# Optimization experiments

Hardware: AMD Instinct MI355X
Metric: run time of the kernel (lower is better)

The kernel has to match this reference:

```python
import jax, jax.numpy as jnp
import numpy as np
from jax import lax

B, T = 64, 256
V, E, H, O = 50000, 256, 512, 50

def _xavier(key, shape):
    fan_in, fan_out = shape[1], shape[0]
    std = float(np.sqrt(2.0 / (fan_in + fan_out)))
    return jax.random.normal(key, shape, dtype=jnp.float32) * std

def lstm_scan(x, W_ih, W_hh, b, h0, c0):
    # x: (B, T, Din); precompute input projection for all timesteps
    xg = jnp.einsum('btd,gd->btg', x, W_ih) + b  # (B, T, 4H)
    def step(carry, xg_t):
        h, c = carry
        g = xg_t + h @ W_hh.T
        i, f, gg, o = jnp.split(g, 4, axis=-1)
        i = jax.nn.sigmoid(i); f = jax.nn.sigmoid(f)
        gg = jnp.tanh(gg); o = jax.nn.sigmoid(o)
        c = f * c + i * gg
        h = o * jnp.tanh(c)
        return (h, c), h
    _, hs = lax.scan(step, (h0, c0), jnp.transpose(xg, (1, 0, 2)))
    return jnp.transpose(hs, (1, 0, 2))  # (B, T, H)

def bilstm(x, W_ih, W_hh, b, h0, c0):
    # Faithful to source bugs: output_backward == output_forward flipped on BATCH dim
    out_f = lstm_scan(x, W_ih, W_hh, b, h0, c0)
    return jnp.concatenate([out_f, out_f[::-1]], axis=-1)  # (B, T, 2H)

def setup_inputs() -> dict:
    key = jax.random.key(0)
    ks = jax.random.split(key, 14)
    x = jax.random.randint(ks[0], (B, T), 0, V + 1, dtype=jnp.int32)
    emb = jax.random.normal(ks[1], (V + 1, E), dtype=jnp.float32)
    emb = emb.at[0].set(0.0)  # padding_idx=0
    s = 1.0 / np.sqrt(H)
    W_ih1 = jax.random.uniform(ks[2], (4 * H, E), minval=-s, maxval=s, dtype=jnp.float32)
    W_hh1 = jax.random.uniform(ks[3], (4 * H, H), minval=-s, maxval=s, dtype=jnp.float32)
    b1 = jax.random.uniform(ks[4], (4 * H,), minval=-s, maxval=s, dtype=jnp.float32)
    W_ih2 = jax.random.uniform(ks[5], (4 * H, 2 * H), minval=-s, maxval=s, dtype=jnp.float32)
    W_hh2 = jax.random.uniform(ks[6], (4 * H, H), minval=-s, maxval=s, dtype=jnp.float32)
    b2 = jax.random.uniform(ks[7], (4 * H,), minval=-s, maxval=s, dtype=jnp.float32)
    h01 = _xavier(ks[8], (B, H)); c01 = _xavier(ks[9], (B, H))
    h02 = _xavier(ks[10], (B, H)); c02 = _xavier(ks[11], (B, H))
    Wfc = jax.random.normal(ks[12], (O, 2 * H), dtype=jnp.float32) * 0.02
    bfc = jnp.zeros((O,), dtype=jnp.float32)
    return {"x": x, "emb": emb, "W_ih1": W_ih1, "W_hh1": W_hh1, "b1": b1,
            "h01": h01, "c01": c01, "W_ih2": W_ih2, "W_hh2": W_hh2, "b2": b2,
            "h02": h02, "c02": c02, "Wfc": Wfc, "bfc": bfc}

def reference(x, emb, W_ih1, W_hh1, b1, h01, c01, W_ih2, W_hh2, b2, h02, c02, Wfc, bfc):
    out = emb[x]                                   # (B, T, E) embedding lookup
    out = bilstm(out, W_ih1, W_hh1, b1, h01, c01)  # (B, T, 2H)
    out = bilstm(out, W_ih2, W_hh2, b2, h02, c02)  # (B, T, 2H)
    # dropout is identity at inference
    logits = jnp.einsum('btd,od->bto', out, Wfc) + bfc
    return jax.nn.log_softmax(logits, axis=-1)
```

## Files before the change

kernel.cpp:

```cpp
#include <hip/hip_runtime.h>


#define B_ 64
#define T_ 256
#define E_ 256
#define H_ 512
#define G_ 2048
#define O_ 50
#define NROW (B_ * T_)
#define RING 16

typedef unsigned short u16;
typedef unsigned int u32;
typedef unsigned long long u64;
typedef short bf16x8 __attribute__((ext_vector_type(8)));
typedef u16 u16x4 __attribute__((ext_vector_type(4)));
typedef u32 u32x4 __attribute__((ext_vector_type(4)));
typedef float f32x4 __attribute__((ext_vector_type(4)));

#define LD_AG(p)    __hip_atomic_load((p), __ATOMIC_RELAXED, __HIP_MEMORY_SCOPE_AGENT)
#define ST_AG(p, v) __hip_atomic_store((p), (v), __ATOMIC_RELAXED, __HIP_MEMORY_SCOPE_AGENT)

__device__ __forceinline__ u16 f2bf(float f) {
    unsigned u = __float_as_uint(f);
    return (u16)((u + 0x7fffu + ((u >> 16) & 1u)) >> 16);
}
__device__ __forceinline__ float bf2f(u16 x) {
    return __uint_as_float(((u32)x) << 16);
}
__device__ __forceinline__ float sigm(float x) {
    x = fminf(fmaxf(x, -30.f), 30.f);
    return 1.f / (1.f + __expf(-x));
}
__device__ __forceinline__ float tanh_f(float x) {
    x = fminf(fmaxf(x, -15.f), 15.f);
    float e = __expf(2.f * x);
    return (e - 1.f) / (e + 1.f);
}
__device__ __forceinline__ bf16x8 pack8(const float* p) {
    float4 v0 = *(const float4*)p;
    float4 v1 = *(const float4*)(p + 4);
    bf16x8 bb;
    bb[0] = (short)f2bf(v0.x); bb[1] = (short)f2bf(v0.y);
    bb[2] = (short)f2bf(v0.z); bb[3] = (short)f2bf(v0.w);
    bb[4] = (short)f2bf(v1.x); bb[5] = (short)f2bf(v1.y);
    bb[6] = (short)f2bf(v1.z); bb[7] = (short)f2bf(v1.w);
    return bb;
}


__global__ __launch_bounds__(256) void f32_to_bf16_vec(
    const float* __restrict__ in, u16* __restrict__ out, int n4)
{
    int i = blockIdx.x * 256 + threadIdx.x;
    if (i >= n4) return;
    float4 v = *(const float4*)&in[(size_t)i * 4];
    u16x4 o = { f2bf(v.x), f2bf(v.y), f2bf(v.z), f2bf(v.w) };
    *(u16x4*)&out[(size_t)i * 4] = o;
}

__global__ __launch_bounds__(256) void embed_to_bf16(
    const int* __restrict__ x, const float* __restrict__ emb, u16* __restrict__ A1)
{
    int i = blockIdx.x * 256 + threadIdx.x;
    int r = i >> 6, c4 = (i & 63) * 4;
    int xi = x[r];
    float4 v = *(const float4*)&emb[(size_t)xi * E_ + c4];
    u16x4 o = { f2bf(v.x), f2bf(v.y), f2bf(v.z), f2bf(v.w) };
    *(u16x4*)&A1[(size_t)r * E_ + c4] = o;
}

__global__ __launch_bounds__(256) void wfc_pad(
    const float* __restrict__ Wfc, u16* __restrict__ outp)
{
    int i = blockIdx.x * 256 + threadIdx.x;
    int row = i >> 8, c4 = (i & 255) * 4;
    u16x4 o = { 0, 0, 0, 0 };
    if (row < O_) {
        float4 v = *(const float4*)&Wfc[(size_t)row * 1024 + c4];
        o = u16x4{ f2bf(v.x), f2bf(v.y), f2bf(v.z), f2bf(v.w) };
    }
    *(u16x4*)&outp[(size_t)row * 1024 + c4] = o;
}

__global__ __launch_bounds__(256) void gemm_bf16(
    const u16* __restrict__ A, const u16* __restrict__ Bw,
    const float* __restrict__ bias, u16* __restrict__ C,
    int M, int N, int K)
{
    __shared__ u16 Asm[128][40];
    __shared__ u16 Bsm[128][40];
    const int tid = threadIdx.x, lane = tid & 63, wave = tid >> 6;
    const int wr = wave >> 1, wc = wave & 1;
    const int bm = blockIdx.y, bn = blockIdx.x;
    f32x4 acc[4][4] = {};
    const int r = tid >> 1, kc = (tid & 1) * 16;
    const u16* ag = A  + (size_t)(bm * 128 + r) * K;
    const u16* bg = Bw + (size_t)(bn * 128 + r) * K;
    for (int k0 = 0; k0 < K; k0 += 32) {
        int col = k0 + kc;
        __syncthreads();
        *(int4*)&Asm[r][kc]     = *(const int4*)(ag + col);
        *(int4*)&Asm[r][kc + 8] = *(const int4*)(ag + col + 8);
        *(int4*)&Bsm[r][kc]     = *(const int4*)(bg + col);
        *(int4*)&Bsm[r][kc + 8] = *(const int4*)(bg + col + 8);
        __syncthreads();
        bf16x8 af[4], bf[4];
        #pragma unroll
        for (int mt = 0; mt < 4; mt++)
            af[mt] = *(const bf16x8*)&Asm[wr * 64 + mt * 16 + (lane & 15)][(lane >> 4) * 8];
        #pragma unroll
        for (int nt = 0; nt < 4; nt++)
            bf[nt] = *(const bf16x8*)&Bsm[wc * 64 + nt * 16 + (lane & 15)][(lane >> 4) * 8];
        #pragma unroll
        for (int mt = 0; mt < 4; mt++)
            #pragma unroll
            for (int nt = 0; nt < 4; nt++)
                acc[mt][nt] = __builtin_amdgcn_mfma_f32_16x16x32_bf16(
                    af[mt], bf[nt], acc[mt][nt], 0, 0, 0);
    }
    #pragma unroll
    for (int mt = 0; mt < 4; mt++) {
        #pragma unroll
        for (int nt = 0; nt < 4; nt++) {
            int col = bn * 128 + wc * 64 + nt * 16 + (lane & 15);
            float bv = bias[col];
            #pragma unroll
            for (int rr = 0; rr < 4; rr++) {
                int row = bm * 128 + wr * 64 + mt * 16 + (lane >> 4) * 4 + rr;
                C[(size_t)row * N + col] = f2bf(acc[mt][nt][rr] + bv);
            }
        }
    }
}

__global__ __launch_bounds__(512, 2) void scan12(
    const u16* __restrict__ xgb,
    const float* __restrict__ Whh1,
    const float* __restrict__ h01, const float* __restrict__ c01,
    u32* h1pub,
    u32* hx1,
    const float* __restrict__ Wih2,
    const float* __restrict__ Whh2,
    const float* __restrict__ b2,
    const float* __restrict__ h02, const float* __restrict__ c02,
    u32* ring,
    u32* hx2,
    u32* h2pk,
    int* sents)
{
    __shared__ u16 hl[16][520];
    __shared__ u16 a1cat[16][1032];
    __shared__ float glds[4][8][68];
    const int tid = threadIdx.x, lane = tid & 63, wave = tid >> 6;
    const int idx = blockIdx.x;
    const u64 tmask = 0xffff0000ffff0000ull;
    int budget = 1 << 20;

    if (idx < 64) {
        const int grp = idx & 7, ug = idx >> 3;
        const int gw = wave >> 1, uh = wave & 1;
        for (int j = tid; j < 8 * 260; j += 512) {
            int rw = 8 + j / 260, cl = (j % 260) * 2;
            *(u32*)&hl[rw][cl] = 0;
        }
        bf16x8 breg0[16], breg1[16];
        #pragma unroll
        for (int tt = 0; tt < 2; tt++) {
            const float* wr0 = Whh1
                + (size_t)(gw * H_ + ug * 64 + uh * 32 + tt * 16 + (lane & 15)) * H_
                + ((lane >> 4) * 8);
            #pragma unroll
            for (int kk = 0; kk < 16; kk++) {
                bf16x8 bb = pack8(wr0 + kk * 32);
                if (tt == 0) breg0[kk] = bb; else breg1[kk] = bb;
            }
        }
        const int bb_ = tid >> 6, uu = tid & 63;
        const int brow = grp * 8 + bb_, ucol = ug * 64 + uu;
        float c = c01[brow * H_ + ucol];
        #pragma unroll
        for (int j = 0; j < 8; ++j) {
            int k = tid + j * 512;
            int prow = k >> 9, pcol = k & 511;
            ST_AG(hx1 + (size_t)(grp * 8 + prow) * H_ + pcol,
                  (1u << 16) | (u32)f2bf(h01[(grp * 8 + prow) * H_ + pcol]));
        }
        const int crow = tid >> 6, ccol = (tid & 63) * 8;
        int* mysent = sents + grp * 32 + ug;
        __syncthreads();

        #pragma unroll 1
        for (int t = 0; t < T_; ++t) {
            const size_t xb = ((size_t)brow * T_ + t) * G_ + ucol;
            u16 xi = xgb[xb], xf = xgb[xb + 512];
            u16 xgg = xgb[xb + 1024], xo = xgb[xb + 1536];

            u64* src = (u64*)(hx1 + (size_t)(t & 1) * (B_ * H_)
                              + (size_t)(grp * 8 + crow) * H_ + ccol);
            const u32 wt = (u32)(t + 1);
            const u64 want = ((u64)wt << 16) | ((u64)wt << 48);
            u64 v0 = LD_AG(src + 0), v1 = LD_AG(src + 1);
            u64 v2 = LD_AG(src + 2), v3 = LD_AG(src + 3);
            while ((((v0 ^ want) | (v1 ^ want) | (v2 ^ want) | (v3 ^ want)) & tmask) != 0) {
                if (--budget < 0) break;
                __builtin_amdgcn_s_sleep(1);
                if ((v0 ^ want) & tmask) v0 = LD_AG(src + 0);
                if ((v1 ^ want) & tmask) v1 = LD_AG(src + 1);
                if ((v2 ^ want) & tmask) v2 = LD_AG(src + 2);
                if ((v3 ^ want) & tmask) v3 = LD_AG(src + 3);
            }
            u32x4 pk = { (u32)(v0 & 0xffff) | ((u32)(v0 >> 32) << 16),
                         (u32)(v1 & 0xffff) | ((u32)(v1 >> 32) << 16),
                         (u32)(v2 & 0xffff) | ((u32)(v2 >> 32) << 16),
                         (u32)(v3 & 0xffff) | ((u32)(v3 >> 32) << 16) };
            *(u32x4*)&hl[crow][ccol] = pk;
            __syncthreads();

            f32x4 a0 = {0,0,0,0}, a1 = {0,0,0,0}, a2 = {0,0,0,0}, a3 = {0,0,0,0};
            const int ar = lane & 15, ac = (lane >> 4) * 8;
            #pragma unroll
            for (int kk = 0; kk < 16; kk += 2) {
                bf16x8 f0 = *(const bf16x8*)&hl[ar][ac + kk * 32];
                bf16x8 f1 = *(const bf16x8*)&hl[ar][ac + (kk + 1) * 32];
                a0 = __builtin_amdgcn_mfma_f32_16x16x32_bf16(f0, breg0[kk],     a0, 0, 0, 0);
                a1 = __builtin_amdgcn_mfma_f32_16x16x32_bf16(f1, breg0[kk + 1], a1, 0, 0, 0);
                a2 = __builtin_amdgcn_mfma_f32_16x16x32_bf16(f0, breg1[kk],     a2, 0, 0, 0);
                a3 = __builtin_amdgcn_mfma_f32_16x16x32_bf16(f1, breg1[kk + 1], a3, 0, 0, 0);
            }
            #pragma unroll
            for (int rr = 0; rr < 4; rr++) {
                int br = (lane >> 4) * 4 + rr;
                if (br < 8) {
                    glds[gw][br][uh * 32 + (lane & 15)]      = a0[rr] + a1[rr];
                    glds[gw][br][uh * 32 + 16 + (lane & 15)] = a2[rr] + a3[rr];
                }
            }
            __syncthreads();

            float ip = glds[0][bb_][uu] + bf2f(xi);
            float fp = glds[1][bb_][uu] + bf2f(xf);
            float gp = glds[2][bb_][uu] + bf2f(xgg);
            float op = glds[3][bb_][uu] + bf2f(xo);
            float gi = sigm(ip), gf = sigm(fp), gc = tanh_f(gp), go = sigm(op);
            c = gf * c + gi * gc;
            float h = go * tanh_f(c);
            u32 me = f2bf(h);
            ST_AG(hx1 + (size_t)((t + 1) & 1) * (B_ * H_) + (size_t)brow * H_ + ucol,
                  ((u32)(t + 2) << 16) | me);
            u32 ot = (u32)__shfl_xor((int)me, 1);
            if (!(uu & 1))
                ST_AG(h1pub + ((size_t)brow * T_ + t) * 256 + (ucol >> 1),
                      me | (ot << 16));
            if (tid == 0) ST_AG(mysent, t + 1);
        }
        __syncthreads();
        if (tid == 0) ST_AG(mysent, T_ + 1);

    } else if (idx < 192) {
        const int bg = idx & 7, gg = (idx - 64) >> 3;
        for (int j = tid; j < 8 * 516; j += 512) {
            int rw = 8 + j / 516, cl = (j % 516) * 2;
            *(u32*)&a1cat[rw][cl] = 0;
        }
        const int gcol = gg * 128 + wave * 16 + (lane & 15);
        bf16x8 bi[32];
        {
            const float* wr0 = Wih2 + (size_t)gcol * 1024 + ((lane >> 4) * 8);
            #pragma unroll
            for (int kk = 0; kk < 32; kk++) bi[kk] = pack8(wr0 + kk * 32);
        }
        const float bias = b2[gcol];
        const int crow = tid >> 6, ccol = (tid & 63) * 16;
        const int myb  = bg * 8 + crow;
        const int myfb = (7 - bg) * 8 + (7 - crow);
        const u32* __restrict__ hbase =
            h1pub + (size_t)((ccol < 512) ? myb : myfb) * T_ * 256;
        const int  cadj  = (ccol < 512) ? (ccol >> 1) : ((ccol - 512) >> 1);
        __syncthreads();

        #pragma unroll 1
        for (int t = 0; t < T_; ++t) {
            if (tid < 16) {
                int g2 = (tid < 8) ? bg : (7 - bg);
                int* sp = sents + g2 * 32 + (tid & 7);
                const int want = t + 2;
                while (LD_AG(sp) < want) {
                    if (--budget < 0) break;
                    __builtin_amdgcn_s_sleep(2);
                }
            } else if (tid < 24 && t >= RING) {
                int* sp = sents + 512 + bg * 32 + (tid - 16);
                const int want = t - (RING - 1);
                while (LD_AG(sp) < want) {
                    if (--budget < 0) break;
                    __builtin_amdgcn_s_sleep(2);
                }
            }
            __syncthreads();

            const u32* s0 = hbase + (size_t)t * 256 + cadj;
            u32x4 q0 = *(const u32x4*)(s0);
            u32x4 q1 = *(const u32x4*)(s0 + 4);
            *(u32x4*)&a1cat[crow][ccol]     = q0;
            *(u32x4*)&a1cat[crow][ccol + 8] = q1;
            __syncthreads();

            f32x4 a0 = {0,0,0,0}, a1 = {0,0,0,0}, a2 = {0,0,0,0}, a3 = {0,0,0,0};
            const int ar = lane & 15, ac = (lane >> 4) * 8;
            #pragma unroll
            for (int kk = 0; kk < 32; kk += 4) {
                bf16x8 f0 = *(const bf16x8*)&a1cat[ar][ac + kk * 32];
                bf16x8 f1 = *(const bf16x8*)&a1cat[ar][ac + (kk + 1) * 32];
                bf16x8 f2 = *(const bf16x8*)&a1cat[ar][ac + (kk + 2) * 32];
                bf16x8 f3 = *(const bf16x8*)&a1cat[ar][ac + (kk + 3) * 32];
                a0 = __builtin_amdgcn_mfma_f32_16x16x32_bf16(f0, bi[kk],     a0, 0, 0, 0);
                a1 = __builtin_amdgcn_mfma_f32_16x16x32_bf16(f1, bi[kk + 1], a1, 0, 0, 0);
                a2 = __builtin_amdgcn_mfma_f32_16x16x32_bf16(f2, bi[kk + 2], a2, 0, 0, 0);
                a3 = __builtin_amdgcn_mfma_f32_16x16x32_bf16(f3, bi[kk + 3], a3, 0, 0, 0);
            }
            #pragma unroll
            for (int rr = 0; rr < 4; rr++) {
                int br = (lane >> 4) * 4 + rr;
                u32 me = f2bf((a0[rr] + a1[rr]) + (a2[rr] + a3[rr]) + bias);
                u32 ot = (u32)__shfl_xor((int)me, 1);
                if (br < 8 && !(lane & 1))
                    ST_AG(ring + ((size_t)(t & (RING - 1)) * B_ + bg * 8 + br) * 1024
                          + (gcol >> 1), me | (ot << 16));
            }
            __syncthreads();
            if (tid == 0) ST_AG(sents + 256 + bg * 32 + gg, t + 1);
        }

    } else {
        const int bg = idx & 7, ug = (idx - 192) >> 3;
        const int gw = wave >> 1, uh = wave & 1;
        for (int j = tid; j < 8 * 260; j += 512) {
            int rw = 8 + j / 260, cl = (j % 260) * 2;
            *(u32*)&hl[rw][cl] = 0;
        }
        bf16x8 breg0[16], breg1[16];
        #pragma unroll
        for (int tt = 0; tt < 2; tt++) {
            const float* wr0 = Whh2
                + (size_t)(gw * H_ + ug * 64 + uh * 32 + tt * 16 + (lane & 15)) * H_
                + ((lane >> 4) * 8);
            #pragma unroll
            for (int kk = 0; kk < 16; kk++) {
                bf16x8 bb = pack8(wr0 + kk * 32);
                if (tt == 0) breg0[kk] = bb; else breg1[kk] = bb;
            }
        }
        const int bb_ = tid >> 6, uu = tid & 63;
        const int brow = bg * 8 + bb_, ucol = ug * 64 + uu;
        float c = c02[brow * H_ + ucol];
        #pragma unroll
        for (int j = 0; j < 8; ++j) {
            int k = tid + j * 512;
            int prow = k >> 9, pcol = k & 511;
            ST_AG(hx2 + (size_t)(bg * 8 + prow) * H_ + pcol,
                  (1u << 16) | (u32)f2bf(h02[(bg * 8 + prow) * H_ + pcol]));
        }
        const int crow = tid >> 6, ccol = (tid & 63) * 8;
        __syncthreads();

        #pragma unroll 1
        for (int t = 0; t < T_; ++t) {
            if (tid < 16) {
                int* sp = sents + 256 + bg * 32 + tid;
                const int want = t + 1;
                while (LD_AG(sp) < want) {
                    if (--budget < 0) break;
                    __builtin_amdgcn_s_sleep(2);
                }
            }
            u64* src = (u64*)(hx2 + (size_t)(t & 1) * (B_ * H_)
                              + (size_t)(bg * 8 + crow) * H_ + ccol);
            const u32 wt = (u32)(t + 1);
            const u64 want = ((u64)wt << 16) | ((u64)wt << 48);
            u64 v0 = LD_AG(src + 0), v1 = LD_AG(src + 1);
            u64 v2 = LD_AG(src + 2), v3 = LD_AG(src + 3);
            while ((((v0 ^ want) | (v1 ^ want) | (v2 ^ want) | (v3 ^ want)) & tmask) != 0) {
                if (--budget < 0) break;
                __builtin_amdgcn_s_sleep(1);
                if ((v0 ^ want) & tmask) v0 = LD_AG(src + 0);
                if ((v1 ^ want) & tmask) v1 = LD_AG(src + 1);
                if ((v2 ^ want) & tmask) v2 = LD_AG(src + 2);
                if ((v3 ^ want) & tmask) v3 = LD_AG(src + 3);
            }
            u32x4 pk = { (u32)(v0 & 0xffff) | ((u32)(v0 >> 32) << 16),
                         (u32)(v1 & 0xffff) | ((u32)(v1 >> 32) << 16),
                         (u32)(v2 & 0xffff) | ((u32)(v2 >> 32) << 16),
                         (u32)(v3 & 0xffff) | ((u32)(v3 >> 32) << 16) };
            *(u32x4*)&hl[crow][ccol] = pk;
            __syncthreads();

            const size_t rb = ((size_t)(t & (RING - 1)) * B_ + brow) * 1024
                              + ug * 32 + (uu >> 1);
            u32 x0 = LD_AG(ring + rb);
            u32 x1 = LD_AG(ring + rb + 256);
            u32 x2 = LD_AG(ring + rb + 512);
            u32 x3 = LD_AG(ring + rb + 768);

            f32x4 a0 = {0,0,0,0}, a1 = {0,0,0,0}, a2 = {0,0,0,0}, a3 = {0,0,0,0};
            const int ar = lane & 15, ac = (lane >> 4) * 8;
            #pragma unroll
            for (int kk = 0; kk < 16; kk += 2) {
                bf16x8 f0 = *(const bf16x8*)&hl[ar][ac + kk * 32];
                bf16x8 f1 = *(const bf16x8*)&hl[ar][ac + (kk + 1) * 32];
                a0 = __builtin_amdgcn_mfma_f32_16x16x32_bf16(f0, breg0[kk],     a0, 0, 0, 0);
                a1 = __builtin_amdgcn_mfma_f32_16x16x32_bf16(f1, breg0[kk + 1], a1, 0, 0, 0);
                a2 = __builtin_amdgcn_mfma_f32_16x16x32_bf16(f0, breg1[kk],     a2, 0, 0, 0);
                a3 = __builtin_amdgcn_mfma_f32_16x16x32_bf16(f1, breg1[kk + 1], a3, 0, 0, 0);
            }
            #pragma unroll
            for (int rr = 0; rr < 4; rr++) {
                int br = (lane >> 4) * 4 + rr;
                if (br < 8) {
                    glds[gw][br][uh * 32 + (lane & 15)]      = a0[rr] + a1[rr];
                    glds[gw][br][uh * 32 + 16 + (lane & 15)] = a2[rr] + a3[rr];
                }
            }
            __syncthreads();
            if (tid == 0) ST_AG(sents + 512 + bg * 32 + ug, t + 1);

            const int sh = (uu & 1) * 16;
            float ip = glds[0][bb_][uu] + bf2f((u16)(x0 >> sh));
            float fp = glds[1][bb_][uu] + bf2f((u16)(x1 >> sh));
            float gp = glds[2][bb_][uu] + bf2f((u16)(x2 >> sh));
            float op = glds[3][bb_][uu] + bf2f((u16)(x3 >> sh));
            float gi = sigm(ip), gf = sigm(fp), gc = tanh_f(gp), go = sigm(op);
            c = gf * c + gi * gc;
            float h = go * tanh_f(c);
            u32 me = f2bf(h);
            ST_AG(hx2 + (size_t)((t + 1) & 1) * (B_ * H_) + (size_t)brow * H_ + ucol,
                  ((u32)(t + 2) << 16) | me);
            u32 ot = (u32)__shfl_xor((int)me, 1);
            if (!(uu & 1))
                h2pk[((size_t)brow * T_ + t) * 256 + (ucol >> 1)] = me | (ot << 16);
        }
    }
}

__global__ __launch_bounds__(256) void fc_mfma(
    const u16* __restrict__ h2, const u16* __restrict__ Wfcp,
    const float* __restrict__ bfc, float* __restrict__ out)
{
    __shared__ u16 hl[16][1032];
    __shared__ float cl[16][68];
    const int tid = threadIdx.x, lane = tid & 63, wave = tid >> 6;
    const int r0 = blockIdx.x * 16;
    const int b = r0 >> 8;
    const int fr0 = (63 - b) * T_ + (r0 & 255);
    #pragma unroll
    for (int j = 0; j < 16; ++j) {
        int k = tid + j * 256;
        int row = k >> 8, c4 = k & 255;
        const u16* src = (c4 < 128)
            ? h2 + (size_t)(r0 + row) * H_ + c4 * 4
            : h2 + (size_t)(fr0 + row) * H_ + (c4 - 128) * 4;
        *(u64*)&hl[row][c4 * 4] = *(const u64*)src;
    }
    __syncthreads();
    const int ar = lane & 15, ac = (lane >> 4) * 8;
    const u16* wrow = Wfcp + (size_t)(wave * 16 + ar) * 1024 + ac;
    f32x4 a0 = {0,0,0,0}, a1 = {0,0,0,0};
    #pragma unroll
    for (int kk = 0; kk < 32; kk += 2) {
        bf16x8 f0 = *(const bf16x8*)&hl[ar][ac + kk * 32];
        bf16x8 f1 = *(const bf16x8*)&hl[ar][ac + (kk + 1) * 32];
        bf16x8 w0 = *(const bf16x8*)(wrow + kk * 32);
        bf16x8 w1 = *(const bf16x8*)(wrow + (kk + 1) * 32);
        a0 = __builtin_amdgcn_mfma_f32_16x16x32_bf16(f0, w0, a0, 0, 0, 0);
        a1 = __builtin_amdgcn_mfma_f32_16x16x32_bf16(f1, w1, a1, 0, 0, 0);
    }
    #pragma unroll
    for (int rr = 0; rr < 4; rr++)
        cl[(lane >> 4) * 4 + rr][wave * 16 + ar] = a0[rr] + a1[rr];
    __syncthreads();
    #pragma unroll
    for (int rr2 = 0; rr2 < 4; rr2++) {
        int row = wave * 4 + rr2;
        float acc = (lane < O_) ? cl[row][lane] + bfc[lane] : -1e30f;
        float m = acc;
        #pragma unroll
        for (int off = 32; off > 0; off >>= 1) m = fmaxf(m, __shfl_xor(m, off));
        float e = (lane < O_) ? __expf(acc - m) : 0.f;
        float sm = e;
        #pragma unroll
        for (int off = 32; off > 0; off >>= 1) sm += __shfl_xor(sm, off);
        float lse = m + __logf(sm);
        if (lane < O_) out[(size_t)(r0 + row) * O_ + lane] = acc - lse;
    }
}


extern "C" void kernel_launch(void* const* d_in, const int* in_sizes, int n_in,
                              void* d_out, int out_size, void* d_ws, size_t ws_size,
                              hipStream_t stream)
{
    (void)in_sizes; (void)n_in; (void)out_size;
    const int*   x    = (const int*)  d_in[0];
    const float* emb  = (const float*)d_in[1];
    const float* Wih1 = (const float*)d_in[2];
    const float* Whh1 = (const float*)d_in[3];
    const float* b1   = (const float*)d_in[4];
    const float* h01  = (const float*)d_in[5];
    const float* c01  = (const float*)d_in[6];
    const float* Wih2 = (const float*)d_in[7];
    const float* Whh2 = (const float*)d_in[8];
    const float* b2   = (const float*)d_in[9];
    const float* h02  = (const float*)d_in[10];
    const float* c02  = (const float*)d_in[11];
    const float* Wfc  = (const float*)d_in[12];
    const float* bfc  = (const float*)d_in[13];
    float* out = (float*)d_out;

    char* ws = (char*)d_ws;
    size_t off = 0;
    auto alloc = [&](size_t bytes) {
        char* p = ws + off; off += (bytes + 255) & ~(size_t)255; return p;
    };
    u16* A1    = (u16*)alloc((size_t)NROW * E_ * 2);
    u16* Wb1   = (u16*)alloc((size_t)G_ * E_ * 2);
    u16* Wfcp  = (u16*)alloc((size_t)64 * 1024 * 2);
    u16* xgb   = (u16*)alloc((size_t)NROW * G_ * 2);
    u32* h1pub = (u32*)alloc((size_t)NROW * 256 * 4);
    u32* ring  = (u32*)alloc((size_t)RING * B_ * 1024 * 4);
    u32* hx1   = (u32*)alloc((size_t)2 * B_ * H_ * 4);
    u32* hx2   = (u32*)alloc((size_t)2 * B_ * H_ * 4);
    u32* h2pk  = (u32*)alloc((size_t)NROW * 256 * 4);
    int* sents = (int*)alloc(768 * sizeof(int));
    if (off > ws_size) return;

    hipMemsetAsync(sents, 0, 768 * sizeof(int), stream);
    f32_to_bf16_vec<<<(G_ * E_ / 4 + 255) / 256, 256, 0, stream>>>(Wih1, Wb1, G_ * E_ / 4);
    wfc_pad<<<64, 256, 0, stream>>>(Wfc, Wfcp);
    embed_to_bf16<<<NROW * E_ / 4 / 256, 256, 0, stream>>>(x, emb, A1);

    gemm_bf16<<<dim3(G_ / 128, NROW / 128), 256, 0, stream>>>(
        A1, Wb1, b1, xgb, NROW, G_, E_);

    scan12<<<256, 512, 0, stream>>>(xgb, Whh1, h01, c01, h1pub, hx1,
                                    Wih2, Whh2, b2, h02, c02, ring, hx2, h2pk,
                                    sents);

    fc_mfma<<<NROW / 16, 256, 0, stream>>>((const u16*)h2pk, Wfcp, bfc, out);
}
```

Before: 909.2 us.

## Fuse embedding gather and bf16 conversion into input GEMM; spin before sleeping

```diff
diff --git a/kernel.cpp b/kernel.cpp
--- a/kernel.cpp
+++ b/kernel.cpp
@@ -48,28 +48,6 @@
     return bb;
 }
 
-
-__global__ __launch_bounds__(256) void f32_to_bf16_vec(
-    const float* __restrict__ in, u16* __restrict__ out, int n4)
-{
-    int i = blockIdx.x * 256 + threadIdx.x;
-    if (i >= n4) return;
-    float4 v = *(const float4*)&in[(size_t)i * 4];
-    u16x4 o = { f2bf(v.x), f2bf(v.y), f2bf(v.z), f2bf(v.w) };
-    *(u16x4*)&out[(size_t)i * 4] = o;
-}
-
-__global__ __launch_bounds__(256) void embed_to_bf16(
-    const int* __restrict__ x, const float* __restrict__ emb, u16* __restrict__ A1)
-{
-    int i = blockIdx.x * 256 + threadIdx.x;
-    int r = i >> 6, c4 = (i & 63) * 4;
-    int xi = x[r];
-    float4 v = *(const float4*)&emb[(size_t)xi * E_ + c4];
-    u16x4 o = { f2bf(v.x), f2bf(v.y), f2bf(v.z), f2bf(v.w) };
-    *(u16x4*)&A1[(size_t)r * E_ + c4] = o;
-}
-
 __global__ __launch_bounds__(256) void wfc_pad(
     const float* __restrict__ Wfc, u16* __restrict__ outp)
 {
@@ -83,10 +61,10 @@
     *(u16x4*)&outp[(size_t)row * 1024 + c4] = o;
 }
 
-__global__ __launch_bounds__(256) void gemm_bf16(
-    const u16* __restrict__ A, const u16* __restrict__ Bw,
-    const float* __restrict__ bias, u16* __restrict__ C,
-    int M, int N, int K)
+__global__ __launch_bounds__(256) void gemm_fused(
+    const int* __restrict__ x, const float* __restrict__ emb,
+    const float* __restrict__ Wih1, const float* __restrict__ b1,
+    u16* __restrict__ C)
 {
     __shared__ u16 Asm[128][40];
     __shared__ u16 Bsm[128][40];
@@ -95,15 +73,17 @@
     const int bm = blockIdx.y, bn = blockIdx.x;
     f32x4 acc[4][4] = {};
     const int r = tid >> 1, kc = (tid & 1) * 16;
-    const u16* ag = A  + (size_t)(bm * 128 + r) * K;
-    const u16* bg = Bw + (size_t)(bn * 128 + r) * K;
-    for (int k0 = 0; k0 < K; k0 += 32) {
+    const int grow = bm * 128 + r;
+    const int xi = x[grow];
+    const float* ag = emb  + (size_t)xi * E_;
+    const float* bg = Wih1 + (size_t)(bn * 128 + r) * E_;
+    for (int k0 = 0; k0 < E_; k0 += 32) {
         int col = k0 + kc;
         __syncthreads();
-        *(int4*)&Asm[r][kc]     = *(const int4*)(ag + col);
-        *(int4*)&Asm[r][kc + 8] = *(const int4*)(ag + col + 8);
-        *(int4*)&Bsm[r][kc]     = *(const int4*)(bg + col);
-        *(int4*)&Bsm[r][kc + 8] = *(const int4*)(bg + col + 8);
+        *(bf16x8*)&Asm[r][kc]     = pack8(ag + col);
+        *(bf16x8*)&Asm[r][kc + 8] = pack8(ag + col + 8);
+        *(bf16x8*)&Bsm[r][kc]     = pack8(bg + col);
+        *(bf16x8*)&Bsm[r][kc + 8] = pack8(bg + col + 8);
         __syncthreads();
         bf16x8 af[4], bf[4];
         #pragma unroll
@@ -124,11 +104,11 @@
         #pragma unroll
         for (int nt = 0; nt < 4; nt++) {
             int col = bn * 128 + wc * 64 + nt * 16 + (lane & 15);
-            float bv = bias[col];
+            float bv = b1[col];
             #pragma unroll
             for (int rr = 0; rr < 4; rr++) {
                 int row = bm * 128 + wr * 64 + mt * 16 + (lane >> 4) * 4 + rr;
-                C[(size_t)row * N + col] = f2bf(acc[mt][nt][rr] + bv);
+                C[(size_t)row * G_ + col] = f2bf(acc[mt][nt][rr] + bv);
             }
         }
     }
@@ -202,9 +182,10 @@
             const u64 want = ((u64)wt << 16) | ((u64)wt << 48);
             u64 v0 = LD_AG(src + 0), v1 = LD_AG(src + 1);
             u64 v2 = LD_AG(src + 2), v3 = LD_AG(src + 3);
+            int spin = 0;
             while ((((v0 ^ want) | (v1 ^ want) | (v2 ^ want) | (v3 ^ want)) & tmask) != 0) {
                 if (--budget < 0) break;
-                __builtin_amdgcn_s_sleep(1);
+                if (++spin > 2) __builtin_amdgcn_s_sleep(1);
                 if ((v0 ^ want) & tmask) v0 = LD_AG(src + 0);
                 if ((v1 ^ want) & tmask) v1 = LD_AG(src + 1);
                 if ((v2 ^ want) & tmask) v2 = LD_AG(src + 2);
@@ -285,16 +266,18 @@
                 int g2 = (tid < 8) ? bg : (7 - bg);
                 int* sp = sents + g2 * 32 + (tid & 7);
                 const int want = t + 2;
+                int spin = 0;
                 while (LD_AG(sp) < want) {
                     if (--budget < 0) break;
-                    __builtin_amdgcn_s_sleep(2);
+                    if (++spin > 2) __builtin_amdgcn_s_sleep(2);
                 }
             } else if (tid < 24 && t >= RING) {
                 int* sp = sents + 512 + bg * 32 + (tid - 16);
                 const int want = t - (RING - 1);
+                int spin = 0;
                 while (LD_AG(sp) < want) {
                     if (--budget < 0) break;
-                    __builtin_amdgcn_s_sleep(2);
+                    if (++spin > 2) __builtin_amdgcn_s_sleep(2);
                 }
             }
             __syncthreads();
@@ -369,9 +352,10 @@
             if (tid < 16) {
                 int* sp = sents + 256 + bg * 32 + tid;
                 const int want = t + 1;
+                int spin = 0;
                 while (LD_AG(sp) < want) {
                     if (--budget < 0) break;
-                    __builtin_amdgcn_s_sleep(2);
+                    if (++spin > 2) __builtin_amdgcn_s_sleep(2);
                 }
             }
             u64* src = (u64*)(hx2 + (size_t)(t & 1) * (B_ * H_)
@@ -380,9 +364,10 @@
             const u64 want = ((u64)wt << 16) | ((u64)wt << 48);
             u64 v0 = LD_AG(src + 0), v1 = LD_AG(src + 1);
             u64 v2 = LD_AG(src + 2), v3 = LD_AG(src + 3);
+            int spin = 0;
             while ((((v0 ^ want) | (v1 ^ want) | (v2 ^ want) | (v3 ^ want)) & tmask) != 0) {
                 if (--budget < 0) break;
-                __builtin_amdgcn_s_sleep(1);
+                if (++spin > 2) __builtin_amdgcn_s_sleep(1);
                 if ((v0 ^ want) & tmask) v0 = LD_AG(src + 0);
                 if ((v1 ^ want) & tmask) v1 = LD_AG(src + 1);
                 if ((v2 ^ want) & tmask) v2 = LD_AG(src + 2);
@@ -521,8 +506,6 @@
     auto alloc = [&](size_t bytes) {
         char* p = ws + off; off += (bytes + 255) & ~(size_t)255; return p;
     };
-    u16* A1    = (u16*)alloc((size_t)NROW * E_ * 2);
-    u16* Wb1   = (u16*)alloc((size_t)G_ * E_ * 2);
     u16* Wfcp  = (u16*)alloc((size_t)64 * 1024 * 2);
     u16* xgb   = (u16*)alloc((size_t)NROW * G_ * 2);
     u32* h1pub = (u32*)alloc((size_t)NROW * 256 * 4);
@@ -534,12 +517,10 @@
     if (off > ws_size) return;
 
     hipMemsetAsync(sents, 0, 768 * sizeof(int), stream);
-    f32_to_bf16_vec<<<(G_ * E_ / 4 + 255) / 256, 256, 0, stream>>>(Wih1, Wb1, G_ * E_ / 4);
     wfc_pad<<<64, 256, 0, stream>>>(Wfc, Wfcp);
-    embed_to_bf16<<<NROW * E_ / 4 / 256, 256, 0, stream>>>(x, emb, A1);
-
-    gemm_bf16<<<dim3(G_ / 128, NROW / 128), 256, 0, stream>>>(
-        A1, Wb1, b1, xgb, NROW, G_, E_);
+
+    gemm_fused<<<dim3(G_ / 128, NROW / 128), 256, 0, stream>>>(
+        x, emb, Wih1, b1, xgb);
 
     scan12<<<256, 512, 0, stream>>>(xgb, Whh1, h01, c01, h1pub, hx1,
                                     Wih2, Whh2, b2, h02, c02, ring, hx2, h2pk,
```

Measured after the change: 878.1 us (median of 2 runs). -3.4%, faster.
